# Performance work log

Hardware: AMD Instinct MI355X
Metric: run time of the kernel (lower is better)

Reference implementation:

```python
import jax, jax.numpy as jnp
import numpy as np
import math

N_LEVELS = 8
PLANE_RES = 512
FEAT_DIM = 16
N_VERT = 10
N_SAMPLES = 262144
LEVEL_OFFSET = 0.0


def _projection_matrices():
    # planotic_solid vertices for n_vertices == 10 (half-dodecahedron)
    phi = (1.0 + math.sqrt(5.0)) / 2.0
    verts = np.array([
        [1.0, 1.0, 1.0], [1.0, 1.0, -1.0], [1.0, -1.0, 1.0], [1.0, -1.0, -1.0],
        [0.0, phi, 1.0 / phi], [0.0, phi, -1.0 / phi],
        [1.0 / phi, 0.0, phi], [1.0 / phi, 0.0, -phi],
        [phi, 1.0 / phi, 0.0], [phi, -1.0 / phi, 0.0]], dtype=np.float64)
    verts /= np.linalg.norm(verts, axis=-1, keepdims=True)
    Ps = []
    for a in verts:
        if a[0] != 0 or a[1] != 0:
            p0 = np.array([-a[1], a[0], 0.0])
        else:
            p0 = np.array([0.0, -a[2], a[1]])
        p1 = np.cross(a, p0)
        p0 /= np.linalg.norm(p0)
        p1 /= np.linalg.norm(p1)
        Ps.append(np.stack([p0, p1], axis=0))
    return np.stack(Ps, axis=0).astype(np.float32)  # (V, 2, 3)

P_MATS = _projection_matrices()

# static ripmap geometry: plane (l1, l2) has shape (H = res>>l2, W = res>>l1)
_W = np.array([PLANE_RES >> l for l in range(N_LEVELS)], dtype=np.int32)
_H = _W.copy()
_SIZES = np.array([int(_H[l2]) * int(_W[l1])
                   for l1 in range(N_LEVELS) for l2 in range(N_LEVELS)], dtype=np.int64)
_OFFS = np.concatenate([[0], np.cumsum(_SIZES)[:-1]]).astype(np.int32)


def build_ripmaps_flat(fm):
    """Build the 8x8 anisotropic mip pyramid and pack all planes into one flat buffer.
    fm: (V, H, W, F). Returns (V, total_pixels, F)."""
    flats = []
    base = fm
    for l1 in range(N_LEVELS):
        if l1 > 0:
            base = 0.5 * (base[:, :, 0::2] + base[:, :, 1::2])  # AvgPool (1,2): pool width
        cur = base
        for l2 in range(N_LEVELS):
            if l2 > 0:
                cur = 0.5 * (cur[:, 0::2] + cur[:, 1::2])        # AvgPool (2,1): pool height
            flats.append(cur.reshape(N_VERT, -1, FEAT_DIM))
    return jnp.concatenate(flats, axis=1)


def multi_anisomip_interp(flat, coords, level):
    """flat: (V, T, F) packed ripmaps; coords: (N, V, 2) in [-1, 1];
    level: (N, V, 2) fractional levels in [0, L-1].
    Quadrilinear: bilinear in space x bilinear across the (l1, l2) level grid."""
    W_arr = jnp.asarray(_W)
    H_arr = jnp.asarray(_H)
    off_arr = jnp.asarray(_OFFS)
    vidx = jnp.arange(N_VERT)[None, :]
    lx, ly = level[..., 0], level[..., 1]
    l1f_f = jnp.clip(jnp.floor(lx), 0.0, N_LEVELS - 1)
    l2f_f = jnp.clip(jnp.floor(ly), 0.0, N_LEVELS - 1)
    wx = jnp.clip(lx - l1f_f, 0.0, 1.0)
    wy = jnp.clip(ly - l2f_f, 0.0, 1.0)
    l1f = l1f_f.astype(jnp.int32)
    l2f = l2f_f.astype(jnp.int32)
    l1c = jnp.minimum(l1f + 1, N_LEVELS - 1)
    l2c = jnp.minimum(l2f + 1, N_LEVELS - 1)
    enc = jnp.zeros(coords.shape[:-1] + (FEAT_DIM,), dtype=flat.dtype)
    for l1, wl1 in ((l1f, 1.0 - wx), (l1c, wx)):
        Wl = W_arr[l1]  # (N, V)
        for l2, wl2 in ((l2f, 1.0 - wy), (l2c, wy)):
            Hl = H_arr[l2]
            off = off_arr[l1 * N_LEVELS + l2]
            u = (coords[..., 0] * 0.5 + 0.5) * Wl - 0.5
            v = (coords[..., 1] * 0.5 + 0.5) * Hl - 0.5
            uf = jnp.floor(u)
            vf = jnp.floor(v)
            fu = u - uf
            fv = v - vf
            ix0 = jnp.clip(uf.astype(jnp.int32), 0, Wl - 1)
            ix1 = jnp.clip(uf.astype(jnp.int32) + 1, 0, Wl - 1)
            iy0 = jnp.clip(vf.astype(jnp.int32), 0, Hl - 1)
            iy1 = jnp.clip(vf.astype(jnp.int32) + 1, 0, Hl - 1)
            wl = wl1 * wl2
            for ix, iy, wc in ((ix0, iy0, (1 - fu) * (1 - fv)),
                               (ix1, iy0, fu * (1 - fv)),
                               (ix0, iy1, (1 - fu) * fv),
                               (ix1, iy1, fu * fv)):
                idx = off + iy * Wl + ix  # (N, V) flat pixel index
                enc = enc + (wl * wc)[..., None] * flat[vidx, idx]
    return enc  # (N, V, F)


def setup_inputs() -> dict:
    key = jax.random.key(0)
    k1, k2, k3 = jax.random.split(key, 3)
    means = jax.random.uniform(k1, (N_SAMPLES, 3), minval=-1.0, maxval=1.0, dtype=jnp.float32)
    A = jax.random.normal(k2, (N_SAMPLES, 3, 3), dtype=jnp.float32) * 0.02
    covs = jnp.einsum('nij,nkj->nik', A, A) + 1e-10 * jnp.eye(3, dtype=jnp.float32)
    fm = jax.random.uniform(k3, (N_VERT, PLANE_RES, PLANE_RES, FEAT_DIM),
                            minval=-0.01, maxval=0.01, dtype=jnp.float32)
    return {"means": means, "covs": covs, "fm": fm}


def reference(means, covs, fm):
    P = jnp.asarray(P_MATS)                                   # (V, 2, 3)
    means_proj = jnp.einsum('nd,vcd->nvc', means, P)          # (N, V, 2)
    sig2 = jnp.einsum('vad,nde,vae->nva', P, covs, P)         # diag of P C P^T, (N, V, 2)
    sigmas = jnp.sqrt(jnp.maximum(sig2, 1e-20))
    level = jnp.log2(sigmas) + LEVEL_OFFSET + math.log2(PLANE_RES)
    level = jnp.clip(level, 0.0, N_LEVELS - 1)
    flat = build_ripmaps_flat(fm)
    enc = multi_anisomip_interp(flat, means_proj, level)      # (N, V, F)
    return enc.reshape(means.shape[0], N_VERT * FEAT_DIM)
```

## Files before the change

### kernel.cpp

```cpp
#include <hip/hip_runtime.h>
#include <hip/hip_fp16.h>


#define NV 10
#define FD 16
#define NS 262144
#define HALF_NS 131072
#define PYR_PX 1040400L
#define DUP0_PX 10404000
#define DUP_VPX 57600
#define OFF_PL   351360000L
#define OFF_CNT  393303040L
#define OFF_LIST 393303104L

__constant__ float c_P[NV][2][3] = {
  {{-0.7071067811865476f, 0.7071067811865476f, 0.0f},
   {-0.4082482904638631f,-0.4082482904638631f, 0.8164965809277261f}},
  {{-0.7071067811865476f, 0.7071067811865476f, 0.0f},
   { 0.4082482904638631f, 0.4082482904638631f, 0.8164965809277261f}},
  {{ 0.7071067811865476f, 0.7071067811865476f, 0.0f},
   {-0.4082482904638631f, 0.4082482904638631f, 0.8164965809277261f}},
  {{ 0.7071067811865476f, 0.7071067811865476f, 0.0f},
   { 0.4082482904638631f,-0.4082482904638631f, 0.8164965809277261f}},
  {{-1.0f, 0.0f, 0.0f},
   { 0.0f,-0.3568220897730899f, 0.9341723589627157f}},
  {{-1.0f, 0.0f, 0.0f},
   { 0.0f, 0.3568220897730899f, 0.9341723589627157f}},
  {{ 0.0f, 1.0f, 0.0f},
   {-0.9341723589627157f, 0.0f, 0.3568220897730899f}},
  {{ 0.0f, 1.0f, 0.0f},
   { 0.9341723589627157f, 0.0f, 0.3568220897730899f}},
  {{-0.3568220897730899f, 0.9341723589627157f, 0.0f},
   { 0.0f, 0.0f, 1.0f}},
  {{ 0.3568220897730899f, 0.9341723589627157f, 0.0f},
   { 0.0f, 0.0f, 1.0f}},
};

__constant__ int c_CW[8] = {0, 512, 768, 896, 960, 992, 1008, 1016};

__device__ __forceinline__ int offp_a(int l1, int l2) {
  return 1044480 - (1020 << (10 - l1)) + ((1024 - (1024 >> l2)) << (9 - l1));
}

__device__ __forceinline__ uint4 havg(uint4 a, uint4 c, __half2 hhalf) {
  uint4 res;
  __half2* rr = (__half2*)&res;
  const __half2* ha = (const __half2*)&a;
  const __half2* hc = (const __half2*)&c;
  #pragma unroll
  for (int j = 0; j < 4; ++j) rr[j] = __hmul2(__hadd2(ha[j], hc[j]), hhalf);
  return res;
}

__global__ __launch_bounds__(256) void build_all(const float* __restrict__ fm,
                                                 __half* __restrict__ pyr,
                                                 int* __restrict__ cnt)
{
  __shared__ uint4 ldsA[2048];
  __shared__ uint4 ldsB[1024];
  int bid = blockIdx.x;
  if (bid == 0 && threadIdx.x == 0) *cnt = 0;
  int v = bid >> 8;
  int rem = bid & 255;
  int b = rem >> 2;
  int s = rem & 3;
  int t = threadIdx.x;

  __half* bv = pyr + (long)v * PYR_PX * FD;
  uint4* bv4 = (uint4*)bv;
  const __half2 hhalf = __floats2half2_rn(0.5f, 0.5f);

  {
    const float4* src = (const float4*)(fm +
        (((long)v * 512 + b * 8) * 512 + s * 128) * FD);
    uint2* ldsu2 = (uint2*)ldsA;
    #pragma unroll
    for (int i = 0; i < 16; ++i) {
      int u = t + 256 * i;
      int r = u >> 9;
      int f4 = u & 511;
      int px = f4 >> 2, qq = f4 & 3;
      float4 d = src[(long)r * 2048 + f4];
      __half2 h0 = __floats2half2_rn(d.x, d.y);
      __half2 h1 = __floats2half2_rn(d.z, d.w);
      uint2 val;
      val.x = *(unsigned*)&h0; val.y = *(unsigned*)&h1;
      ldsu2[(r * 128 + px) * 4 + qq] = val;
    }
  }
  __syncthreads();

  #pragma unroll
  for (int l1 = 0; l1 < 8; ++l1) {
    uint4* cur = (l1 & 1) ? ldsB : ldsA;
    const int Wc = 128 >> l1;

    if (l1 < 7) {
      uint4* nxt = (l1 & 1) ? ldsA : ldsB;
      const int Wn = Wc >> 1;
      const int units = 8 * Wn * 2;
      for (int u = t; u < units; u += 256) {
        int k = u & 1;
        int xr = u >> 1;
        int x = xr & (Wn - 1);
        int r = xr >> (6 - l1);
        uint4 a = cur[(r * Wc + 2 * x) * 2 + k];
        uint4 c = cur[(r * Wc + 2 * x + 1) * 2 + k];
        nxt[(r * Wn + x) * 2 + k] = havg(a, c, hhalf);
      }
    }

    if (l1 >= 1) {
      const int slots = Wc * 2;
      if (t < slots) {
        int k = t & 1, x = t >> 1;
        const int Wg = 512 >> l1;
        uint4 r0 = cur[(0 * Wc + x) * 2 + k];
        uint4 r1 = cur[(1 * Wc + x) * 2 + k];
        uint4 r2 = cur[(2 * Wc + x) * 2 + k];
        uint4 r3 = cur[(3 * Wc + x) * 2 + k];
        uint4 r4 = cur[(4 * Wc + x) * 2 + k];
        uint4 r5 = cur[(5 * Wc + x) * 2 + k];
        uint4 r6 = cur[(6 * Wc + x) * 2 + k];
        uint4 r7 = cur[(7 * Wc + x) * 2 + k];
        uint4 a0 = havg(r0, r1, hhalf), a1 = havg(r2, r3, hhalf);
        uint4 a2 = havg(r4, r5, hhalf), a3 = havg(r6, r7, hhalf);
        uint4 b0 = havg(a0, a1, hhalf), b1 = havg(a2, a3, hhalf);
        uint4 c0 = havg(b0, b1, hhalf);
        int gx = s * Wc + x;
        long p1 = (long)offp_a(l1, 1) + (long)(b * 4) * Wg + gx;
        bv4[p1 * 2 + k] = a0;
        bv4[(p1 + Wg) * 2 + k] = a1;
        bv4[(p1 + 2 * Wg) * 2 + k] = a2;
        bv4[(p1 + 3 * Wg) * 2 + k] = a3;
        long p2 = (long)offp_a(l1, 2) + (long)(b * 2) * Wg + gx;
        bv4[p2 * 2 + k] = b0;
        bv4[(p2 + Wg) * 2 + k] = b1;
        long p3 = (long)offp_a(l1, 3) + (long)b * Wg + gx;
        bv4[p3 * 2 + k] = c0;
      }
    }
    __syncthreads();
  }
}

template<int L2SRC, int NLEV>
__global__ __launch_bounds__(256) void pool_hN(__half* __restrict__ pyr)
{
  constexpr int R = 1 << NLEV;
  constexpr int HL = 512 >> (L2SRC + NLEV);
  int total = NV * HL * 1016;
  int t = blockIdx.x * 256 + threadIdx.x;
  if (t >= total) return;
  int u = t % 1016;
  int r2 = t / 1016;
  int c = 512 + (u >> 1), k = u & 1;
  int y = r2 % HL;
  int v = r2 / HL;
  int l1 = 0;
  #pragma unroll
  for (int i = 1; i < 8; ++i) l1 += (c >= c_CW[i]) ? 1 : 0;
  int x = c - c_CW[l1];
  int W = 512 >> l1;
  __half* bv = pyr + (long)v * PYR_PX * FD;
  const __half* src = bv + (long)offp_a(l1, L2SRC) * FD;

  uint4 d[R];
  long base = ((long)(y * R) * W + x) * FD + k * 8;
  #pragma unroll
  for (int r = 0; r < R; ++r)
    d[r] = *(const uint4*)(src + base + (long)r * W * FD);

  const __half2 hhalf = __floats2half2_rn(0.5f, 0.5f);
  #pragma unroll
  for (int lev = 1; lev <= NLEV; ++lev) {
    int cnt = R >> lev;
    __half* dst = bv + (long)offp_a(l1, L2SRC + lev) * FD;
    #pragma unroll
    for (int r = 0; r < cnt; ++r) {
      d[r] = havg(d[2 * r], d[2 * r + 1], hhalf);
      *(uint4*)(dst + (((long)(y * cnt + r)) * W + x) * FD + k * 8) = d[r];
    }
  }
}

__global__ __launch_bounds__(256) void build_dup(__half* __restrict__ pyr)
{
  int cb = blockIdx.y;
  int l1 = 2 + (cb >> 2), l2 = 2 + (cb & 3);
  int W = 512 >> l1, H = 512 >> l2;
  int units = NV * W * H * 2;
  int gx = blockIdx.x * 256 + threadIdx.x;
  if (gx >= units) return;
  int k = gx & 1;
  int p = gx >> 1;
  int x = p & (W - 1);
  int r = p >> (9 - l1);
  int y = r & (H - 1);
  int v = r >> (9 - l2);
  long srcPx = (long)v * PYR_PX + offp_a(l1, l2) + y * W + min(x + 1, W - 1);
  int Ad = 61440 - (245760 >> l1);
  int Bd = 256 - (1024 >> l2);
  long dstPx = (long)DUP0_PX + (long)v * DUP_VPX + Ad + ((Bd + y) << (9 - l1)) + x;
  const uint4* src = (const uint4*)(pyr + srcPx * FD);
  uint4* dst = (uint4*)(pyr + dstPx * FD);
  dst[k] = src[k];
}

__global__ __launch_bounds__(256) void proj_kernel(const float* __restrict__ means,
                                                   const float* __restrict__ covs,
                                                   float4* __restrict__ pl,
                                                   int* __restrict__ cnt,
                                                   int* __restrict__ list)
{
  __shared__ int lbuf[2560];
  __shared__ int lcnt, lbase;
  if (threadIdx.x == 0) lcnt = 0;
  __syncthreads();
  int n = blockIdx.x * 256 + threadIdx.x;
  float m0 = means[3 * n], m1 = means[3 * n + 1], m2 = means[3 * n + 2];
  const float* C = covs + 9L * n;
  float c0 = C[0], c1 = C[1], c2 = C[2];
  float c3 = C[3], c4 = C[4], c5 = C[5];
  float c6 = C[6], c7 = C[7], c8 = C[8];
  #pragma unroll
  for (int v = 0; v < NV; ++v) {
    float p00 = c_P[v][0][0], p01 = c_P[v][0][1], p02 = c_P[v][0][2];
    float p10 = c_P[v][1][0], p11 = c_P[v][1][1], p12 = c_P[v][1][2];
    float cx = m0 * p00 + m1 * p01 + m2 * p02;
    float cy = m0 * p10 + m1 * p11 + m2 * p12;
    float t0 = c0 * p00 + c1 * p01 + c2 * p02;
    float t1 = c3 * p00 + c4 * p01 + c5 * p02;
    float t2 = c6 * p00 + c7 * p01 + c8 * p02;
    float s2x = p00 * t0 + p01 * t1 + p02 * t2;
    t0 = c0 * p10 + c1 * p11 + c2 * p12;
    t1 = c3 * p10 + c4 * p11 + c5 * p12;
    t2 = c6 * p10 + c7 * p11 + c8 * p12;
    float s2y = p10 * t0 + p11 * t1 + p12 * t2;
    float lx = 0.5f * log2f(fmaxf(s2x, 1e-20f)) + 9.0f;
    float ly = 0.5f * log2f(fmaxf(s2y, 1e-20f)) + 9.0f;
    lx = fminf(fmaxf(lx, 0.0f), 7.0f);
    ly = fminf(fmaxf(ly, 0.0f), 7.0f);
    pl[(long)v * NS + n] = make_float4(cx, cy, lx, ly);
    if (lx < 1.0f || ly < 1.0f) {
      int pos = atomicAdd(&lcnt, 1);
      lbuf[pos] = v * NS + n;
    }
  }
  __syncthreads();
  if (threadIdx.x == 0) lbase = atomicAdd(cnt, lcnt);
  __syncthreads();
  for (int i = threadIdx.x; i < lcnt; i += 256) list[lbase + i] = lbuf[i];
}

struct Ctx {
  int oA, oB, oC, oD, oE, oF, oG, oH;
  __half2 wA, wB, wC, wD, wE, wF, wG, wH;
};

__device__ __forceinline__ Ctx mk_ctx(const float4 p, const bool qodd,
                                      const int dupRel)
{
  Ctx c;
  float cx = p.x, cy = p.y, lx = p.z, ly = p.w;
  int l1f = (int)lx, l2f = (int)ly;
  float wx = lx - (float)l1f, wy = ly - (float)l2f;
  int l1c = min(l1f + 1, 7);
  int l2c = min(l2f + 1, 7);

  int sh_0 = 9 - l1f;
  int Ar_0 = 1044480 - (1020 << (10 - l1f));
  float u0 = (cx * 0.5f + 0.5f) * (float)(1 << sh_0) - 0.5f;
  float uf0 = floorf(u0);
  float fu0 = u0 - uf0;
  int iu0 = (int)uf0;
  bool e0 = (iu0 < 0) || (iu0 >= (1 << sh_0) - 1);
  int ix_0 = min(max(iu0, 0), (1 << sh_0) - 1);
  float wxl_0 = qodd ? (e0 ? 0.0f : fu0) : (e0 ? 1.0f : 1.0f - fu0);
  int pOdd_0 = ix_0 & 1;
  int Ad_0 = 61440 - (245760 >> l1f);
  int inR1_0 = ((unsigned)(l1f - 2) <= 3u) ? 1 : 0;

  int sh_1 = 9 - l1c;
  int Ar_1 = 1044480 - (1020 << (10 - l1c));
  float u1 = (cx * 0.5f + 0.5f) * (float)(1 << sh_1) - 0.5f;
  float uf1 = floorf(u1);
  float fu1 = u1 - uf1;
  int iu1 = (int)uf1;
  bool e1 = (iu1 < 0) || (iu1 >= (1 << sh_1) - 1);
  int ix_1 = min(max(iu1, 0), (1 << sh_1) - 1);
  float wxl_1 = qodd ? (e1 ? 0.0f : fu1) : (e1 ? 1.0f : 1.0f - fu1);
  int pOdd_1 = ix_1 & 1;
  int Ad_1 = 61440 - (245760 >> l1c);
  int inR1_1 = ((unsigned)(l1c - 2) <= 3u) ? 1 : 0;

  float wl1_0 = 1.0f - wx, wl1_1 = wx;

  int H0 = 512 >> l2f;
  float vv0 = (cy * 0.5f + 0.5f) * (float)H0 - 0.5f;
  float vf0 = floorf(vv0);
  float fv_0 = vv0 - vf0;
  int iv0 = (int)vf0;
  int iy_0 = min(max(iv0, 0), H0 - 1);
  int dy_0 = min(max(iv0 + 1, 0), H0 - 1) - iy_0;
  int Bv_0 = 1024 - (1024 >> l2f);
  int Bd_0 = 256 - (1024 >> l2f);
  int inR2_0 = ((unsigned)(l2f - 2) <= 3u) ? 1 : 0;

  int H1 = 512 >> l2c;
  float vv1 = (cy * 0.5f + 0.5f) * (float)H1 - 0.5f;
  float vf1 = floorf(vv1);
  float fv_1 = vv1 - vf1;
  int iv1 = (int)vf1;
  int iy_1 = min(max(iv1, 0), H1 - 1);
  int dy_1 = min(max(iv1 + 1, 0), H1 - 1) - iy_1;
  int Bv_1 = 1024 - (1024 >> l2c);
  int Bd_1 = 256 - (1024 >> l2c);
  int inR2_1 = ((unsigned)(l2c - 2) <= 3u) ? 1 : 0;

  float wl2_0 = 1.0f - wy, wl2_1 = wy;

  bool s00 = pOdd_0 && inR1_0 && inR2_0;
  c.oA = s00 ? (dupRel + Ad_0 + ((Bd_0 + iy_0) << sh_0) + ix_0 - 1)
             : (Ar_0 + ((Bv_0 + iy_0) << sh_0) + ix_0);
  c.oB = c.oA + (dy_0 << sh_0);
  bool s01 = pOdd_0 && inR1_0 && inR2_1;
  c.oC = s01 ? (dupRel + Ad_0 + ((Bd_1 + iy_1) << sh_0) + ix_0 - 1)
             : (Ar_0 + ((Bv_1 + iy_1) << sh_0) + ix_0);
  c.oD = c.oC + (dy_1 << sh_0);
  bool s10 = pOdd_1 && inR1_1 && inR2_0;
  c.oE = s10 ? (dupRel + Ad_1 + ((Bd_0 + iy_0) << sh_1) + ix_1 - 1)
             : (Ar_1 + ((Bv_0 + iy_0) << sh_1) + ix_1);
  c.oF = c.oE + (dy_0 << sh_1);
  bool s11 = pOdd_1 && inR1_1 && inR2_1;
  c.oG = s11 ? (dupRel + Ad_1 + ((Bd_1 + iy_1) << sh_1) + ix_1 - 1)
             : (Ar_1 + ((Bv_1 + iy_1) << sh_1) + ix_1);
  c.oH = c.oG + (dy_1 << sh_1);

  float wb00 = wl1_0 * wl2_0 * wxl_0;
  float wb01 = wl1_0 * wl2_1 * wxl_0;
  float wb10 = wl1_1 * wl2_0 * wxl_1;
  float wb11 = wl1_1 * wl2_1 * wxl_1;
  c.wA = __float2half2_rn(wb00 * (1.0f - fv_0));
  c.wB = __float2half2_rn(wb00 * fv_0);
  c.wC = __float2half2_rn(wb01 * (1.0f - fv_1));
  c.wD = __float2half2_rn(wb01 * fv_1);
  c.wE = __float2half2_rn(wb10 * (1.0f - fv_0));
  c.wF = __float2half2_rn(wb10 * fv_0);
  c.wG = __float2half2_rn(wb11 * (1.0f - fv_1));
  c.wH = __float2half2_rn(wb11 * fv_1);

  __half2 z = __float2half2_rn(0.0f);
  if (l1f == 0) { c.wA = z; c.wB = z; c.wC = z; c.wD = z; }
  if (l2f == 0) { c.wA = z; c.wB = z; c.wE = z; c.wF = z; }
  return c;
}

__global__ __launch_bounds__(256) void interp8(const float4* __restrict__ pl,
                                               const __half* __restrict__ pyr,
                                               float* __restrict__ out)
{
  int bid = blockIdx.x;
  int swz = (bid & 7) * 2560 + (bid >> 3);
  int t = swz * 256 + threadIdx.x;
  int q = t & 3;
  bool qodd = (q & 1);
  int vlow = (t >> 2) & 1;
  int n = (t >> 3) & (HALF_NS - 1);
  int v2 = t >> 20;
  int v = v2 * 2 + vlow;
  int nA = n, nB = n + HALF_NS;
  int dupRel = DUP0_PX + v * DUP_VPX - v * 1040400;

  float4 pA = pl[(long)v * NS + nA];
  float4 pB = pl[(long)v * NS + nB];

  const __half* bvq = pyr + (long)v * PYR_PX * FD + ((q & 1) * 16 + (q >> 1) * 8);

  Ctx cA = mk_ctx(pA, qodd, dupRel);
  uint4 dAA = *(const uint4*)(bvq + (long)cA.oA * FD);
  uint4 dAB = *(const uint4*)(bvq + (long)cA.oB * FD);
  uint4 dAC = *(const uint4*)(bvq + (long)cA.oC * FD);
  uint4 dAD = *(const uint4*)(bvq + (long)cA.oD * FD);
  uint4 dAE = *(const uint4*)(bvq + (long)cA.oE * FD);
  uint4 dAF = *(const uint4*)(bvq + (long)cA.oF * FD);
  uint4 dAG = *(const uint4*)(bvq + (long)cA.oG * FD);
  uint4 dAH = *(const uint4*)(bvq + (long)cA.oH * FD);

  Ctx cB = mk_ctx(pB, qodd, dupRel);
  uint4 dBA = *(const uint4*)(bvq + (long)cB.oA * FD);
  uint4 dBB = *(const uint4*)(bvq + (long)cB.oB * FD);
  uint4 dBC = *(const uint4*)(bvq + (long)cB.oC * FD);
  uint4 dBD = *(const uint4*)(bvq + (long)cB.oD * FD);
  uint4 dBE = *(const uint4*)(bvq + (long)cB.oE * FD);
  uint4 dBF = *(const uint4*)(bvq + (long)cB.oF * FD);
  uint4 dBG = *(const uint4*)(bvq + (long)cB.oG * FD);
  uint4 dBH = *(const uint4*)(bvq + (long)cB.oH * FD);
  __builtin_amdgcn_sched_barrier(0);

  __half2 z = __float2half2_rn(0.0f);
  __half2 aA0 = z, aA1 = z, aA2 = z, aA3 = z;
  __half2 aB0 = z, aB1 = z, aB2 = z, aB3 = z;
  #define ACC8(A0, A1, A2, A3, D, W) { const __half2* hh = (const __half2*)&(D); \
    A0 = __hfma2(hh[0], (W), A0); A1 = __hfma2(hh[1], (W), A1);                   \
    A2 = __hfma2(hh[2], (W), A2); A3 = __hfma2(hh[3], (W), A3); }
  ACC8(aA0,aA1,aA2,aA3, dAA, cA.wA) ACC8(aA0,aA1,aA2,aA3, dAB, cA.wB)
  ACC8(aA0,aA1,aA2,aA3, dAC, cA.wC) ACC8(aA0,aA1,aA2,aA3, dAD, cA.wD)
  ACC8(aA0,aA1,aA2,aA3, dAE, cA.wE) ACC8(aA0,aA1,aA2,aA3, dAF, cA.wF)
  ACC8(aA0,aA1,aA2,aA3, dAG, cA.wG) ACC8(aA0,aA1,aA2,aA3, dAH, cA.wH)
  ACC8(aB0,aB1,aB2,aB3, dBA, cB.wA) ACC8(aB0,aB1,aB2,aB3, dBB, cB.wB)
  ACC8(aB0,aB1,aB2,aB3, dBC, cB.wC) ACC8(aB0,aB1,aB2,aB3, dBD, cB.wD)
  ACC8(aB0,aB1,aB2,aB3, dBE, cB.wE) ACC8(aB0,aB1,aB2,aB3, dBF, cB.wF)
  ACC8(aB0,aB1,aB2,aB3, dBG, cB.wG) ACC8(aB0,aB1,aB2,aB3, dBH, cB.wH)
  #undef ACC8

  #define XC(A0, A1, A2, A3) {                                   \
    int x0 = *(int*)&A0, x1 = *(int*)&A1;                        \
    int x2 = *(int*)&A2, x3 = *(int*)&A3;                        \
    int y0 = __shfl_xor(x0, 1), y1 = __shfl_xor(x1, 1);          \
    int y2 = __shfl_xor(x2, 1), y3 = __shfl_xor(x3, 1);          \
    A0 = __hadd2(A0, *(__half2*)&y0); A1 = __hadd2(A1, *(__half2*)&y1); \
    A2 = __hadd2(A2, *(__half2*)&y2); A3 = __hadd2(A3, *(__half2*)&y3); }
  XC(aA0, aA1, aA2, aA3)
  XC(aB0, aB1, aB2, aB3)
  #undef XC

  __half2 sA0 = qodd ? aA2 : aA0;
  __half2 sA1 = qodd ? aA3 : aA1;
  float2 fA0 = __half22float2(sA0);
  float2 fA1 = __half22float2(sA1);
  *(float4*)(out + ((long)nA * NV + v) * FD + q * 4) =
      make_float4(fA0.x, fA0.y, fA1.x, fA1.y);

  __half2 sB0 = qodd ? aB2 : aB0;
  __half2 sB1 = qodd ? aB3 : aB1;
  float2 fB0 = __half22float2(sB0);
  float2 fB1 = __half22float2(sB1);
  *(float4*)(out + ((long)nB * NV + v) * FD + q * 4) =
      make_float4(fB0.x, fB0.y, fB1.x, fB1.y);
}

__global__ __launch_bounds__(256) void fixup2(const float4* __restrict__ pl,
                                              const __half* __restrict__ pyr,
                                              const float* __restrict__ fm,
                                              const int* __restrict__ cnt,
                                              const int* __restrict__ list,
                                              float* __restrict__ out)
{
  int nfix = *cnt;
  int lane = threadIdx.x & 63;
  int wid = (blockIdx.x * 256 + threadIdx.x) >> 6;
  int nw = (gridDim.x * 256) >> 6;
  int k  = lane & 1;
  int h  = (lane >> 1) & 1;
  int xs = (lane >> 2) & 1;
  int r  = (lane >> 3) & 1;
  int jj = (lane >> 4) & 1;
  int ii = (lane >> 5) & 1;

  for (int idx = wid; idx < nfix; idx += nw) {
    int pv = list[idx];
    int v = pv >> 18, n = pv & (NS - 1);
    float4 p = pl[(long)pv];
    float cx = p.x, cy = p.y, lx = p.z, ly = p.w;
    int l1f = (int)lx, l2f = (int)ly;
    float wx = lx - (float)l1f, wy = ly - (float)l2f;
    int l1 = ii ? min(l1f + 1, 7) : l1f;
    int l2 = jj ? min(l2f + 1, 7) : l2f;
    float wl1 = ii ? wx : 1.0f - wx;
    float wl2 = jj ? wy : 1.0f - wy;
    int Wl = 512 >> l1, Hl = 512 >> l2;

    float u = (cx * 0.5f + 0.5f) * (float)Wl - 0.5f;
    float uf = floorf(u);
    float fu = u - uf;
    int iu = (int)uf;
    int ix0 = min(max(iu, 0), Wl - 1);
    int ix1 = min(max(iu + 1, 0), Wl - 1);
    int ix = xs ? ix1 : ix0;
    float wxs = xs ? fu : 1.0f - fu;

    float vv = (cy * 0.5f + 0.5f) * (float)Hl - 0.5f;
    float vf = floorf(vv);
    float fv = vv - vf;
    int iv = (int)vf;
    int iy0 = min(max(iv, 0), Hl - 1);
    int iy1 = min(max(iv + 1, 0), Hl - 1);
    int iy = r ? iy1 : iy0;
    float wys = r ? fv : 1.0f - fv;

    float w = wl1 * wl2 * wxs * wys;
    float s0=0,s1=0,s2=0,s3=0,s4=0,s5=0,s6=0,s7=0;

    const float* fmb = fm + (long)v * (262144L * FD) + h * 8;
    if (l1 > 0 && l2 > 0) {
      if (k == 0) {
        const __half* pp = pyr + ((long)v * PYR_PX + offp_a(l1, l2) +
                                  (long)iy * Wl + ix) * FD + h * 8;
        uint4 d = *(const uint4*)pp;
        const __half2* hh = (const __half2*)&d;
        float2 f0 = __half22float2(hh[0]), f1 = __half22float2(hh[1]);
        float2 f2 = __half22float2(hh[2]), f3 = __half22float2(hh[3]);
        s0=f0.x; s1=f0.y; s2=f1.x; s3=f1.y; s4=f2.x; s5=f2.y; s6=f3.x; s7=f3.y;
      }
    } else if (l1 == 0 && l2 == 0) {
      if (k == 0) {
        const float* s = fmb + ((long)iy * 512 + ix) * FD;
        float4 g0 = *(const float4*)s, g1 = *(const float4*)(s + 4);
        s0=g0.x; s1=g0.y; s2=g0.z; s3=g0.w; s4=g1.x; s5=g1.y; s6=g1.z; s7=g1.w;
      }
    } else if (l2 == 0) {
      int m = 1 << l1, base = ix << l1;
      for (int e = k; e < m; e += 2) {
        const float* s = fmb + ((long)iy * 512 + base + e) * FD;
        float4 g0 = *(const float4*)s, g1 = *(const float4*)(s + 4);
        s0+=g0.x; s1+=g0.y; s2+=g0.z; s3+=g0.w;
        s4+=g1.x; s5+=g1.y; s6+=g1.z; s7+=g1.w;
      }
      float inv = 1.0f / (float)m;
      s0*=inv; s1*=inv; s2*=inv; s3*=inv; s4*=inv; s5*=inv; s6*=inv; s7*=inv;
    } else {
      int m = 1 << l2, base = iy << l2;
      for (int e = k; e < m; e += 2) {
        const float* s = fmb + ((long)(base + e) * 512 + ix) * FD;
        float4 g0 = *(const float4*)s, g1 = *(const float4*)(s + 4);
        s0+=g0.x; s1+=g0.y; s2+=g0.z; s3+=g0.w;
        s4+=g1.x; s5+=g1.y; s6+=g1.z; s7+=g1.w;
      }
      float inv = 1.0f / (float)m;
      s0*=inv; s1*=inv; s2*=inv; s3*=inv; s4*=inv; s5*=inv; s6*=inv; s7*=inv;
    }

    float a0=w*s0, a1=w*s1, a2=w*s2, a3=w*s3;
    float a4=w*s4, a5=w*s5, a6=w*s6, a7=w*s7;

    #define RED(M) { a0 += __shfl_xor(a0, M); a1 += __shfl_xor(a1, M); \
      a2 += __shfl_xor(a2, M); a3 += __shfl_xor(a3, M);                \
      a4 += __shfl_xor(a4, M); a5 += __shfl_xor(a5, M);                \
      a6 += __shfl_xor(a6, M); a7 += __shfl_xor(a7, M); }
    RED(1) RED(4) RED(8) RED(16) RED(32)
    #undef RED

    if (lane == 0 || lane == 2) {
      float* o = out + ((long)n * NV + v) * FD + h * 8;
      *(float4*)o = make_float4(a0, a1, a2, a3);
      *(float4*)(o + 4) = make_float4(a4, a5, a6, a7);
    }
  }
}

extern "C" void kernel_launch(void* const* d_in, const int* in_sizes, int n_in,
                              void* d_out, int out_size, void* d_ws, size_t ws_size,
                              hipStream_t stream)
{
  const float* means = (const float*)d_in[0];
  const float* covs  = (const float*)d_in[1];
  const float* fm    = (const float*)d_in[2];
  float* out = (float*)d_out;
  __half* pyr = (__half*)d_ws;
  float4* pl  = (float4*)((char*)d_ws + OFF_PL);
  int* cnt    = (int*)((char*)d_ws + OFF_CNT);
  int* list   = (int*)((char*)d_ws + OFF_LIST);

  build_all<<<NV * 256, 256, 0, stream>>>(fm, pyr, cnt);
  {
    int tB = NV * 4 * 1016;
    pool_hN<3, 4><<<(tB + 255) / 256, 256, 0, stream>>>(pyr);
  }
  {
    dim3 g(1280, 16, 1);
    build_dup<<<g, 256, 0, stream>>>(pyr);
  }
  proj_kernel<<<NS / 256, 256, 0, stream>>>(means, covs, pl, cnt, list);

  interp8<<<20480, 256, 0, stream>>>(pl, pyr, out);
  fixup2<<<4096, 256, 0, stream>>>(pl, pyr, fm, cnt, list, out);
}
```

Baseline: 237.2 us.

## Fuse projection into pyramid build, emit dup planes inline, segment fixup lists

Folds the projection/level kernel into the pyramid build launch as extra blocks, and writes the shifted duplicate planes directly from build_all and pool_hN instead of running a separate build_dup kernel that re-reads the pyramid. The global atomic counter is replaced by per-block fixed-size list segments with per-segment counts, and fixup2 assigns four waves per segment. This removes two launches and a read-back pass at the cost of extra scattered stores in the build kernels and possible load imbalance across fixup segments.

Result: slower. 253.3 us (+6.8%).

```diff
diff --git a/kernel.cpp b/kernel.cpp
--- a/kernel.cpp
+++ b/kernel.cpp
@@ -10,8 +10,8 @@
 #define DUP0_PX 10404000
 #define DUP_VPX 57600
 #define OFF_PL   351360000L
-#define OFF_CNT  393303040L
 #define OFF_LIST 393303104L
+#define OFF_CNTS 403788864L
 
 __constant__ float c_P[NV][2][3] = {
   {{-0.7071067811865476f, 0.7071067811865476f, 0.0f},
@@ -54,21 +54,68 @@
 
 __global__ __launch_bounds__(256) void build_all(const float* __restrict__ fm,
                                                  __half* __restrict__ pyr,
-                                                 int* __restrict__ cnt)
+                                                 const float* __restrict__ means,
+                                                 const float* __restrict__ covs,
+                                                 float4* __restrict__ pl,
+                                                 int* __restrict__ list,
+                                                 int* __restrict__ cnts)
 {
   __shared__ uint4 ldsA[2048];
   __shared__ uint4 ldsB[1024];
+  __shared__ int lcnt;
   int bid = blockIdx.x;
-  if (bid == 0 && threadIdx.x == 0) *cnt = 0;
+  int t = threadIdx.x;
+
+  if (bid >= NV * 256) {
+    int b2 = bid - NV * 256;
+    int* lbuf = (int*)ldsA;
+    if (t == 0) lcnt = 0;
+    __syncthreads();
+    int n = b2 * 256 + t;
+    float m0 = means[3 * n], m1 = means[3 * n + 1], m2 = means[3 * n + 2];
+    const float* C = covs + 9L * n;
+    float c0 = C[0], c1 = C[1], c2 = C[2];
+    float c3 = C[3], c4 = C[4], c5 = C[5];
+    float c6 = C[6], c7 = C[7], c8 = C[8];
+    #pragma unroll
+    for (int v = 0; v < NV; ++v) {
+      float p00 = c_P[v][0][0], p01 = c_P[v][0][1], p02 = c_P[v][0][2];
+      float p10 = c_P[v][1][0], p11 = c_P[v][1][1], p12 = c_P[v][1][2];
+      float cx = m0 * p00 + m1 * p01 + m2 * p02;
+      float cy = m0 * p10 + m1 * p11 + m2 * p12;
+      float t0 = c0 * p00 + c1 * p01 + c2 * p02;
+      float t1 = c3 * p00 + c4 * p01 + c5 * p02;
+      float t2 = c6 * p00 + c7 * p01 + c8 * p02;
+      float s2x = p00 * t0 + p01 * t1 + p02 * t2;
+      t0 = c0 * p10 + c1 * p11 + c2 * p12;
+      t1 = c3 * p10 + c4 * p11 + c5 * p12;
+      t2 = c6 * p10 + c7 * p11 + c8 * p12;
+      float s2y = p10 * t0 + p11 * t1 + p12 * t2;
+      float lx = 0.5f * log2f(fmaxf(s2x, 1e-20f)) + 9.0f;
+      float ly = 0.5f * log2f(fmaxf(s2y, 1e-20f)) + 9.0f;
+      lx = fminf(fmaxf(lx, 0.0f), 7.0f);
+      ly = fminf(fmaxf(ly, 0.0f), 7.0f);
+      pl[(long)v * NS + n] = make_float4(cx, cy, lx, ly);
+      if (lx < 1.0f || ly < 1.0f) {
+        int pos = atomicAdd(&lcnt, 1);
+        lbuf[pos] = v * NS + n;
+      }
+    }
+    __syncthreads();
+    if (t == 0) cnts[b2] = lcnt;
+    for (int i = t; i < lcnt; i += 256) list[b2 * 2560 + i] = lbuf[i];
+    return;
+  }
+
   int v = bid >> 8;
   int rem = bid & 255;
   int b = rem >> 2;
   int s = rem & 3;
-  int t = threadIdx.x;
 
   __half* bv = pyr + (long)v * PYR_PX * FD;
   uint4* bv4 = (uint4*)bv;
   const __half2 hhalf = __floats2half2_rn(0.5f, 0.5f);
+  const long dupRel = (long)DUP0_PX + (long)v * DUP_VPX - (long)v * PYR_PX;
 
   {
     const float4* src = (const float4*)(fm +
@@ -138,6 +185,21 @@
         bv4[(p2 + Wg) * 2 + k] = b1;
         long p3 = (long)offp_a(l1, 3) + (long)b * Wg + gx;
         bv4[p3 * 2 + k] = c0;
+
+        if ((unsigned)(l1 - 2) <= 3u) {
+          int Ad = 61440 - (245760 >> l1);
+          int sh = 9 - l1;
+          if (gx >= 1) {
+            bv4[(dupRel + Ad + ((long)(2 * b) << sh) + gx - 1) * 2 + k] = b0;
+            bv4[(dupRel + Ad + ((long)(2 * b + 1) << sh) + gx - 1) * 2 + k] = b1;
+            bv4[(dupRel + Ad + ((long)(128 + b) << sh) + gx - 1) * 2 + k] = c0;
+          }
+          if (gx == Wg - 1) {
+            bv4[(dupRel + Ad + ((long)(2 * b) << sh) + gx) * 2 + k] = b0;
+            bv4[(dupRel + Ad + ((long)(2 * b + 1) << sh) + gx) * 2 + k] = b1;
+            bv4[(dupRel + Ad + ((long)(128 + b) << sh) + gx) * 2 + k] = c0;
+          }
+        }
       }
     }
     __syncthreads();
@@ -164,6 +226,10 @@
   int W = 512 >> l1;
   __half* bv = pyr + (long)v * PYR_PX * FD;
   const __half* src = bv + (long)offp_a(l1, L2SRC) * FD;
+  const long dupRel = (long)DUP0_PX + (long)v * DUP_VPX - (long)v * PYR_PX;
+  bool dupl1 = ((unsigned)(l1 - 2) <= 3u);
+  int Ad = 61440 - (245760 >> l1);
+  int sh = 9 - l1;
 
   uint4 d[R];
   long base = ((long)(y * R) * W + x) * FD + k * 8;
@@ -175,82 +241,22 @@
   #pragma unroll
   for (int lev = 1; lev <= NLEV; ++lev) {
     int cnt = R >> lev;
-    __half* dst = bv + (long)offp_a(l1, L2SRC + lev) * FD;
+    int l2g = L2SRC + lev;
+    __half* dst = bv + (long)offp_a(l1, l2g) * FD;
+    int Bd = 256 - (1024 >> l2g);
     #pragma unroll
     for (int r = 0; r < cnt; ++r) {
       d[r] = havg(d[2 * r], d[2 * r + 1], hhalf);
-      *(uint4*)(dst + (((long)(y * cnt + r)) * W + x) * FD + k * 8) = d[r];
+      int yy = y * cnt + r;
+      *(uint4*)(dst + (((long)yy) * W + x) * FD + k * 8) = d[r];
+      if (dupl1 && l2g <= 5) {
+        if (x >= 1)
+          ((uint4*)bv)[(dupRel + Ad + ((long)(Bd + yy) << sh) + x - 1) * 2 + k] = d[r];
+        if (x == W - 1)
+          ((uint4*)bv)[(dupRel + Ad + ((long)(Bd + yy) << sh) + x) * 2 + k] = d[r];
+      }
     }
   }
-}
-
-__global__ __launch_bounds__(256) void build_dup(__half* __restrict__ pyr)
-{
-  int cb = blockIdx.y;
-  int l1 = 2 + (cb >> 2), l2 = 2 + (cb & 3);
-  int W = 512 >> l1, H = 512 >> l2;
-  int units = NV * W * H * 2;
-  int gx = blockIdx.x * 256 + threadIdx.x;
-  if (gx >= units) return;
-  int k = gx & 1;
-  int p = gx >> 1;
-  int x = p & (W - 1);
-  int r = p >> (9 - l1);
-  int y = r & (H - 1);
-  int v = r >> (9 - l2);
-  long srcPx = (long)v * PYR_PX + offp_a(l1, l2) + y * W + min(x + 1, W - 1);
-  int Ad = 61440 - (245760 >> l1);
-  int Bd = 256 - (1024 >> l2);
-  long dstPx = (long)DUP0_PX + (long)v * DUP_VPX + Ad + ((Bd + y) << (9 - l1)) + x;
-  const uint4* src = (const uint4*)(pyr + srcPx * FD);
-  uint4* dst = (uint4*)(pyr + dstPx * FD);
-  dst[k] = src[k];
-}
-
-__global__ __launch_bounds__(256) void proj_kernel(const float* __restrict__ means,
-                                                   const float* __restrict__ covs,
-                                                   float4* __restrict__ pl,
-                                                   int* __restrict__ cnt,
-                                                   int* __restrict__ list)
-{
-  __shared__ int lbuf[2560];
-  __shared__ int lcnt, lbase;
-  if (threadIdx.x == 0) lcnt = 0;
-  __syncthreads();
-  int n = blockIdx.x * 256 + threadIdx.x;
-  float m0 = means[3 * n], m1 = means[3 * n + 1], m2 = means[3 * n + 2];
-  const float* C = covs + 9L * n;
-  float c0 = C[0], c1 = C[1], c2 = C[2];
-  float c3 = C[3], c4 = C[4], c5 = C[5];
-  float c6 = C[6], c7 = C[7], c8 = C[8];
-  #pragma unroll
-  for (int v = 0; v < NV; ++v) {
-    float p00 = c_P[v][0][0], p01 = c_P[v][0][1], p02 = c_P[v][0][2];
-    float p10 = c_P[v][1][0], p11 = c_P[v][1][1], p12 = c_P[v][1][2];
-    float cx = m0 * p00 + m1 * p01 + m2 * p02;
-    float cy = m0 * p10 + m1 * p11 + m2 * p12;
-    float t0 = c0 * p00 + c1 * p01 + c2 * p02;
-    float t1 = c3 * p00 + c4 * p01 + c5 * p02;
-    float t2 = c6 * p00 + c7 * p01 + c8 * p02;
-    float s2x = p00 * t0 + p01 * t1 + p02 * t2;
-    t0 = c0 * p10 + c1 * p11 + c2 * p12;
-    t1 = c3 * p10 + c4 * p11 + c5 * p12;
-    t2 = c6 * p10 + c7 * p11 + c8 * p12;
-    float s2y = p10 * t0 + p11 * t1 + p12 * t2;
-    float lx = 0.5f * log2f(fmaxf(s2x, 1e-20f)) + 9.0f;
-    float ly = 0.5f * log2f(fmaxf(s2y, 1e-20f)) + 9.0f;
-    lx = fminf(fmaxf(lx, 0.0f), 7.0f);
-    ly = fminf(fmaxf(ly, 0.0f), 7.0f);
-    pl[(long)v * NS + n] = make_float4(cx, cy, lx, ly);
-    if (lx < 1.0f || ly < 1.0f) {
-      int pos = atomicAdd(&lcnt, 1);
-      lbuf[pos] = v * NS + n;
-    }
-  }
-  __syncthreads();
-  if (threadIdx.x == 0) lbase = atomicAdd(cnt, lcnt);
-  __syncthreads();
-  for (int i = threadIdx.x; i < lcnt; i += 256) list[lbase + i] = lbuf[i];
 }
 
 struct Ctx {
@@ -443,14 +449,15 @@
 __global__ __launch_bounds__(256) void fixup2(const float4* __restrict__ pl,
                                               const __half* __restrict__ pyr,
                                               const float* __restrict__ fm,
-                                              const int* __restrict__ cnt,
+                                              const int* __restrict__ cnts,
                                               const int* __restrict__ list,
                                               float* __restrict__ out)
 {
-  int nfix = *cnt;
   int lane = threadIdx.x & 63;
   int wid = (blockIdx.x * 256 + threadIdx.x) >> 6;
-  int nw = (gridDim.x * 256) >> 6;
+  int seg = wid >> 2;
+  int sub = wid & 3;
+  int nfix = cnts[seg];
   int k  = lane & 1;
   int h  = (lane >> 1) & 1;
   int xs = (lane >> 2) & 1;
@@ -458,8 +465,8 @@
   int jj = (lane >> 4) & 1;
   int ii = (lane >> 5) & 1;
 
-  for (int idx = wid; idx < nfix; idx += nw) {
-    int pv = list[idx];
+  for (int idx = sub; idx < nfix; idx += 4) {
+    int pv = list[seg * 2560 + idx];
     int v = pv >> 18, n = pv & (NS - 1);
     float4 p = pl[(long)pv];
     float cx = p.x, cy = p.y, lx = p.z, ly = p.w;
@@ -559,20 +566,15 @@
   float* out = (float*)d_out;
   __half* pyr = (__half*)d_ws;
   float4* pl  = (float4*)((char*)d_ws + OFF_PL);
-  int* cnt    = (int*)((char*)d_ws + OFF_CNT);
   int* list   = (int*)((char*)d_ws + OFF_LIST);
-
-  build_all<<<NV * 256, 256, 0, stream>>>(fm, pyr, cnt);
+  int* cnts   = (int*)((char*)d_ws + OFF_CNTS);
+
+  build_all<<<NV * 256 + 1024, 256, 0, stream>>>(fm, pyr, means, covs,
+                                                 pl, list, cnts);
   {
     int tB = NV * 4 * 1016;
     pool_hN<3, 4><<<(tB + 255) / 256, 256, 0, stream>>>(pyr);
   }
-  {
-    dim3 g(1280, 16, 1);
-    build_dup<<<g, 256, 0, stream>>>(pyr);
-  }
-  proj_kernel<<<NS / 256, 256, 0, stream>>>(means, covs, pl, cnt, list);
-
   interp8<<<20480, 256, 0, stream>>>(pl, pyr, out);
-  fixup2<<<4096, 256, 0, stream>>>(pl, pyr, fm, cnt, list, out);
-}
+  fixup2<<<1024, 256, 0, stream>>>(pl, pyr, fm, cnts, list, out);
+}
```
